# Kernel tuning notes

Hardware: AMD Instinct MI355X
Metric: run time of the kernel (lower is better)

## Reference

```python
import jax, jax.numpy as jnp
import numpy as np

E = 768
NH_REG = 6   # num_heads - cultural_heads
NH_CUL = 2   # cultural_heads


def _branch(x, wq, bq, wk, bk, wv, bv, wo, bo, cb, nh, mask_add):
    # x: [B,T,E]; weights stored as [in,out]; cb: [1,nh,1,hd]
    B, T, Edim = x.shape
    hd = Edim // nh
    scale = hd ** -0.5
    q = (x @ wq + bq).reshape(B, T, nh, hd).transpose(0, 2, 1, 3)
    k = (x @ wk + bk).reshape(B, T, nh, hd).transpose(0, 2, 1, 3)
    v = (x @ wv + bv).reshape(B, T, nh, hd).transpose(0, 2, 1, 3)
    q = q + cb  # learned cultural bias added to Q
    scores = jnp.einsum('bhtd,bhsd->bhts', q, k) * scale
    scores = scores + mask_add
    w = jax.nn.softmax(scores, axis=-1)  # dropout omitted (eval mode)
    out = jnp.einsum('bhts,bhsd->bhtd', w, v)
    out = out.transpose(0, 2, 1, 3).reshape(B, T, Edim)
    return out @ wo + bo


def setup_inputs() -> dict:
    key = jax.random.key(0)
    ks = jax.random.split(key, 24)
    B, S = 2, 2048
    d = {
        'hidden_states': jax.random.normal(ks[0], (B, S, E), jnp.float32),
        'cultural_mask': jax.random.normal(ks[1], (B, S, S), jnp.float32),
        'attention_mask': jax.random.normal(ks[2], (B, 1, 1, S), jnp.float32),
    }
    s = E ** -0.5
    names = ['rq_w', 'rk_w', 'rv_w', 'ro_w', 'cq_w', 'ck_w', 'cv_w', 'co_w']
    for i, n in enumerate(names):
        d[n] = jax.random.normal(ks[3 + i], (E, E), jnp.float32) * s
    for i, n in enumerate(['rq_b', 'rk_b', 'rv_b', 'ro_b', 'cq_b', 'ck_b', 'cv_b', 'co_b']):
        d[n] = jax.random.normal(ks[11 + i], (E,), jnp.float32) * 0.02
    d['r_cb'] = jnp.zeros((1, NH_REG, 1, E // NH_REG), jnp.float32)
    d['c_cb'] = jnp.zeros((1, NH_CUL, 1, E // NH_CUL), jnp.float32)
    # NOTE: concat of two branches gives 2E features -> out layer maps 2E -> E
    d['out_w'] = jax.random.normal(ks[19], (2 * E, E), jnp.float32) * (2 * E) ** -0.5
    d['out_b'] = jax.random.normal(ks[20], (E,), jnp.float32) * 0.02
    return d


def reference(hidden_states, cultural_mask, attention_mask,
              rq_w, rk_w, rv_w, ro_w, cq_w, ck_w, cv_w, co_w,
              rq_b, rk_b, rv_b, ro_b, cq_b, ck_b, cv_b, co_b,
              r_cb, c_cb, out_w, out_b):
    # regular branch: attention_mask only
    reg = _branch(hidden_states, rq_w, rq_b, rk_w, rk_b, rv_w, rv_b,
                  ro_w, ro_b, r_cb, NH_REG, attention_mask)
    # cultural branch: cultural_mask (broadcast over heads) + attention_mask
    cmask = cultural_mask[:, None, :, :] + attention_mask
    cul = _branch(hidden_states, cq_w, cq_b, ck_w, ck_b, cv_w, cv_b,
                  co_w, co_b, c_cb, NH_CUL, cmask)
    combined = jnp.concatenate([reg, cul], axis=-1)  # [B,T,2E]
    return combined @ out_w + out_b
```

## Files before the change

kernel.cpp:

```cpp
#include <hip/hip_runtime.h>
#include <hip/hip_bf16.h>

using u16 = unsigned short;
using u32 = unsigned int;
typedef short short8 __attribute__((ext_vector_type(8)));
typedef float f32x4 __attribute__((ext_vector_type(4)));

#define B_  2
#define S_  2048
#define E_  768
#define BS_ 4096

#define L2E_ 1.44269504088896f
#define FML2_ 17.3123404906676f

__device__ __forceinline__ u16 f2bf(float f) {
  __hip_bfloat16 h = __float2bfloat16(f);
  return *reinterpret_cast<u16*>(&h);
}

__device__ __forceinline__ u32 pk2(float a, float b) {
  return (u32)f2bf(a) | ((u32)f2bf(b) << 16);
}

__device__ __forceinline__ void gld16(const void* g, void* l) {
  __builtin_amdgcn_global_load_lds(
      (const __attribute__((address_space(1))) u32*)g,
      (__attribute__((address_space(3))) u32*)l, 16, 0, 0);
}


__global__ __launch_bounds__(256) void conv_x_k(const float* __restrict__ x,
                                                u16* __restrict__ xb, int n4) {
  int i = blockIdx.x * 256 + threadIdx.x;
  if (i >= n4) return;
  float4 v = reinterpret_cast<const float4*>(x)[i];
  reinterpret_cast<uint2*>(xb)[i] = make_uint2(pk2(v.x, v.y), pk2(v.z, v.w));
}

__global__ __launch_bounds__(256) void bias_k(
    const float* rqb, const float* rkb, const float* rvb,
    const float* cqb, const float* ckb, const float* cvb,
    const float* rob, const float* cob,
    const float* rcb, const float* ccb,
    float* bqkv, float* bproj) {
  int t = blockIdx.x * 256 + threadIdx.x;
  if (t < 4608) {
    int seg = t / 768, i = t - seg * 768;
    float v = 0.f;
    if      (seg == 0) v = rqb[i] + rcb[i];
    else if (seg == 1) v = rkb[i];
    else if (seg == 2) v = rvb[i];
    else if (seg == 3) v = cqb[i] + ccb[i];
    else if (seg == 4) v = ckb[i];
    else               v = cvb[i];
    bqkv[t] = v;
  } else {
    int u = t - 4608;
    if (u < 1536) bproj[u] = (u < 768) ? rob[u] : cob[u - 768];
  }
}

struct TP {
  const float* src[9];
  u16* dst[9];
  int rows[9];
};

__global__ __launch_bounds__(256) void transpose_k(TP p) {
  int mi = blockIdx.z;
  int rows = p.rows[mi];
  int r0 = blockIdx.y * 32;
  if (r0 >= rows) return;
  int c0 = blockIdx.x * 32;
  const float* src = p.src[mi];
  u16* dst = p.dst[mi];
  __shared__ float t[32][33];
  int tx = threadIdx.x & 31, ty = threadIdx.x >> 5;
#pragma unroll
  for (int d = 0; d < 4; ++d) {
    int r = ty + d * 8;
    t[r][tx] = src[(size_t)(r0 + r) * 768 + c0 + tx];
  }
  __syncthreads();
#pragma unroll
  for (int d = 0; d < 4; ++d) {
    int c = ty + d * 8;
    dst[(size_t)(c0 + c) * rows + r0 + tx] = f2bf(t[tx][c]);
  }
}


template<int MODE>
__global__ __launch_bounds__(256) void gemm_t_k(
    const u16* __restrict__ A, int lda,
    const u16* __restrict__ BT, int ldb,
    const float* __restrict__ bias, int K,
    const u16* __restrict__ A2, int msplit, int bofs,
    void* __restrict__ Cout, int ldc,
    u16* __restrict__ Qr, u16* __restrict__ Kr, u16* __restrict__ Vtr,
    u16* __restrict__ Qc, u16* __restrict__ Kc, u16* __restrict__ Vtc) {
  __shared__ u16 lA[128 * 32];
  __shared__ u16 lB[128 * 32];
  const int tid = threadIdx.x, w = tid >> 6, lane = tid & 63;
  const int quad = lane >> 4, l15 = lane & 15;
  const int m0 = blockIdx.y * 128, n0 = blockIdx.x * 128;
  if (msplit && m0 >= msplit) { A = A2 - (size_t)msplit * lda; BT += bofs; }

  const f32x4 z4 = {0.f, 0.f, 0.f, 0.f};
  f32x4 acc[4][4];
#pragma unroll
  for (int i = 0; i < 4; ++i)
#pragma unroll
    for (int j = 0; j < 4; ++j) acc[i][j] = z4;

  const int sr = w * 32 + (lane >> 2);
  const int scp = lane & 3;

  for (int kt = 0; kt < K; kt += 32) {
    int r1 = sr, r2 = sr + 16;
    int c1 = (scp - (r1 >> 2)) & 3;
    int c2 = (scp - (r2 >> 2)) & 3;
    gld16(A + (size_t)(m0 + r1) * lda + kt + c1 * 8, &lA[r1 * 32 + scp * 8]);
    gld16(A + (size_t)(m0 + r2) * lda + kt + c2 * 8, &lA[r2 * 32 + scp * 8]);
    gld16(BT + (size_t)(n0 + r1) * ldb + kt + c1 * 8, &lB[r1 * 32 + scp * 8]);
    gld16(BT + (size_t)(n0 + r2) * ldb + kt + c2 * 8, &lB[r2 * 32 + scp * 8]);
    __syncthreads();
    short8 af[4], bg[4];
#pragma unroll
    for (int i = 0; i < 4; ++i) {
      int r = (w >> 1) * 64 + i * 16 + l15;
      af[i] = *reinterpret_cast<const short8*>(&lA[r * 32 + ((quad + (r >> 2)) & 3) * 8]);
    }
#pragma unroll
    for (int j = 0; j < 4; ++j) {
      int r = (w & 1) * 64 + j * 16 + l15;
      bg[j] = *reinterpret_cast<const short8*>(&lB[r * 32 + ((quad + (r >> 2)) & 3) * 8]);
    }
#pragma unroll
    for (int i = 0; i < 4; ++i)
#pragma unroll
      for (int j = 0; j < 4; ++j)
        acc[i][j] = __builtin_amdgcn_mfma_f32_16x16x32_bf16(af[i], bg[j], acc[i][j], 0, 0, 0);
    __syncthreads();
  }

  const int seg = (MODE == 2) ? (m0 / 768) : 0;
#pragma unroll
  for (int i = 0; i < 4; ++i) {
    int f = m0 + (w >> 1) * 64 + i * 16 + quad * 4;
    float4 b4 = *reinterpret_cast<const float4*>(bias + f);
#pragma unroll
    for (int j = 0; j < 4; ++j) {
      int t = n0 + (w & 1) * 64 + j * 16 + l15;
      float v0 = acc[i][j][0] + b4.x;
      float v1 = acc[i][j][1] + b4.y;
      float v2 = acc[i][j][2] + b4.z;
      float v3 = acc[i][j][3] + b4.w;
      if (MODE == 0) {
        *reinterpret_cast<uint2*>((u16*)Cout + (size_t)t * ldc + f) =
            make_uint2(pk2(v0, v1), pk2(v2, v3));
      } else if (MODE == 1) {
        *reinterpret_cast<float4*>((float*)Cout + (size_t)t * ldc + f) =
            make_float4(v0, v1, v2, v3);
      } else {
        int b = t >> 11, s = t & 2047;
        int fs = f - seg * 768;
        if (seg == 0) {
          int h = fs >> 7, d = fs & 127;
          *reinterpret_cast<uint2*>(Qr + ((size_t)(b * 6 + h) * 2048 + s) * 128 + d) =
              make_uint2(pk2(v0, v1), pk2(v2, v3));
        } else if (seg == 1) {
          int h = fs >> 7, d = fs & 127;
          *reinterpret_cast<uint2*>(Kr + ((size_t)(b * 6 + h) * 2048 + s) * 128 + d) =
              make_uint2(pk2(v0, v1), pk2(v2, v3));
        } else if (seg == 2) {
          int h = fs >> 7, d = fs & 127;
          u16* vp = Vtr + ((size_t)(b * 6 + h) * 128 + d) * 2048 + s;
          vp[0] = f2bf(v0); vp[2048] = f2bf(v1); vp[4096] = f2bf(v2); vp[6144] = f2bf(v3);
        } else if (seg == 3) {
          int h = fs / 384, d = fs - h * 384;
          *reinterpret_cast<uint2*>(Qc + ((size_t)(b * 2 + h) * 2048 + s) * 384 + d) =
              make_uint2(pk2(v0, v1), pk2(v2, v3));
        } else if (seg == 4) {
          int h = fs / 384, d = fs - h * 384;
          *reinterpret_cast<uint2*>(Kc + ((size_t)(b * 2 + h) * 2048 + s) * 384 + d) =
              make_uint2(pk2(v0, v1), pk2(v2, v3));
        } else {
          int h = fs / 384, d = fs - h * 384;
          u16* vp = Vtc + ((size_t)(b * 2 + h) * 384 + d) * 2048 + s;
          vp[0] = f2bf(v0); vp[2048] = f2bf(v1); vp[4096] = f2bf(v2); vp[6144] = f2bf(v3);
        }
      }
    }
  }
}

__global__ __launch_bounds__(256) void attn_g1_k(
    const u16* __restrict__ Qr, const u16* __restrict__ Kr,
    const u16* __restrict__ Qc, const u16* __restrict__ Kc,
    u16* __restrict__ Pr, u16* __restrict__ Pc, float* __restrict__ Lp,
    const float* __restrict__ am, const float* __restrict__ cmask,
    float sReg, float sCul, int zoff) {
  __shared__ u16 lA[128 * 32];
  __shared__ u16 lB[128 * 32];
  const int tid = threadIdx.x, w = tid >> 6, lane = tid & 63;
  const int quad = lane >> 4, l15 = lane & 15;
  const int m0 = blockIdx.y * 128, n0 = blockIdx.x * 128;
  const int gz = zoff + blockIdx.z;
  const u16 *A, *BT;
  u16* P;
  const float* cm = nullptr;
  float scl;
  int K, b;
  if (gz < 12) {
    A = Kr + (size_t)gz * S_ * 128;
    BT = Qr + (size_t)gz * S_ * 128;
    K = 128;
    P = Pr + (size_t)blockIdx.z * (size_t)S_ * S_;
    scl = sReg;
    b = gz / 6;
  } else {
    int hc = gz - 12;
    A = Kc + (size_t)hc * S_ * 384;
    BT = Qc + (size_t)hc * S_ * 384;
    K = 384;
    P = Pc + (size_t)hc * (size_t)S_ * S_;
    b = hc >> 1;
    cm = cmask + (size_t)b * S_ * S_;
    scl = sCul;
  }

  const f32x4 z4 = {0.f, 0.f, 0.f, 0.f};
  f32x4 acc[4][4];
#pragma unroll
  for (int i = 0; i < 4; ++i)
#pragma unroll
    for (int j = 0; j < 4; ++j) acc[i][j] = z4;

  const int sr = w * 32 + (lane >> 2);
  const int scp = lane & 3;

  for (int kt = 0; kt < K; kt += 32) {
    int r1 = sr, r2 = sr + 16;
    int c1 = (scp - (r1 >> 2)) & 3;
    int c2 = (scp - (r2 >> 2)) & 3;
    gld16(A + (size_t)(m0 + r1) * K + kt + c1 * 8, &lA[r1 * 32 + scp * 8]);
    gld16(A + (size_t)(m0 + r2) * K + kt + c2 * 8, &lA[r2 * 32 + scp * 8]);
    gld16(BT + (size_t)(n0 + r1) * K + kt + c1 * 8, &lB[r1 * 32 + scp * 8]);
    gld16(BT + (size_t)(n0 + r2) * K + kt + c2 * 8, &lB[r2 * 32 + scp * 8]);
    __syncthreads();
    short8 af[4], bg[4];
#pragma unroll
    for (int i = 0; i < 4; ++i) {
      int r = (w >> 1) * 64 + i * 16 + l15;
      af[i] = *reinterpret_cast<const short8*>(&lA[r * 32 + ((quad + (r >> 2)) & 3) * 8]);
    }
#pragma unroll
    for (int j = 0; j < 4; ++j) {
      int r = (w & 1) * 64 + j * 16 + l15;
      bg[j] = *reinterpret_cast<const short8*>(&lB[r * 32 + ((quad + (r >> 2)) & 3) * 8]);
    }
#pragma unroll
    for (int i = 0; i < 4; ++i)
#pragma unroll
      for (int j = 0; j < 4; ++j)
        acc[i][j] = __builtin_amdgcn_mfma_f32_16x16x32_bf16(af[i], bg[j], acc[i][j], 0, 0, 0);
    __syncthreads();
  }

  const float* amb = am + b * S_;
  float lsum[4] = {0.f, 0.f, 0.f, 0.f};
#pragma unroll
  for (int i = 0; i < 4; ++i) {
    int kb = m0 + (w >> 1) * 64 + i * 16 + quad * 4;
    float4 a4 = *reinterpret_cast<const float4*>(amb + kb);
    float pre0 = fmaf(a4.x, L2E_, -FML2_);
    float pre1 = fmaf(a4.y, L2E_, -FML2_);
    float pre2 = fmaf(a4.z, L2E_, -FML2_);
    float pre3 = fmaf(a4.w, L2E_, -FML2_);
#pragma unroll
    for (int j = 0; j < 4; ++j) {
      int q = n0 + (w & 1) * 64 + j * 16 + l15;
      float c0 = pre0, c1 = pre1, c2 = pre2, c3 = pre3;
      if (cm) {
        float4 cmv = *reinterpret_cast<const float4*>(cm + (size_t)q * S_ + kb);
        c0 = fmaf(cmv.x, L2E_, c0);
        c1 = fmaf(cmv.y, L2E_, c1);
        c2 = fmaf(cmv.z, L2E_, c2);
        c3 = fmaf(cmv.w, L2E_, c3);
      }
      float p0 = exp2f(fmaf(acc[i][j][0], scl, c0));
      float p1 = exp2f(fmaf(acc[i][j][1], scl, c1));
      float p2 = exp2f(fmaf(acc[i][j][2], scl, c2));
      float p3 = exp2f(fmaf(acc[i][j][3], scl, c3));
      lsum[j] += (p0 + p1) + (p2 + p3);
      *reinterpret_cast<uint2*>(P + (size_t)q * S_ + kb) =
          make_uint2(pk2(p0, p1), pk2(p2, p3));
    }
  }
#pragma unroll
  for (int j = 0; j < 4; ++j) {
    float s = lsum[j];
    s += __shfl_xor(s, 16);
    s += __shfl_xor(s, 32);
    if (lane < 16)
      Lp[(size_t)gz * (32 * S_) + ((size_t)((m0 >> 7) * 2 + (w >> 1))) * S_ +
         n0 + (w & 1) * 64 + j * 16 + lane] = s;
  }
}

__global__ __launch_bounds__(256) void attn_g2_k(
    const u16* __restrict__ Pr, const u16* __restrict__ Pc,
    const u16* __restrict__ Vtr, const u16* __restrict__ Vtc,
    const float* __restrict__ Lp, u16* __restrict__ AO, int zoff) {
  const int gz = zoff + blockIdx.z;
  const int m0 = blockIdx.y * 128, n0 = blockIdx.x * 128;
  const u16 *A, *BT;
  int b, colbase;
  if (gz < 12) {
    if (blockIdx.y) return;
    A = Vtr + (size_t)gz * 128 * S_;
    BT = Pr + (size_t)blockIdx.z * (size_t)S_ * S_;
    b = gz / 6;
    colbase = (gz % 6) * 128;
  } else {
    int hc = gz - 12;
    A = Vtc + (size_t)hc * 384 * S_;
    BT = Pc + (size_t)hc * (size_t)S_ * S_;
    b = hc >> 1;
    colbase = 768 + (hc & 1) * 384;
  }
  __shared__ u16 lA[128 * 32];
  __shared__ u16 lB[128 * 32];
  __shared__ float lL[128];
  const int tid = threadIdx.x, w = tid >> 6, lane = tid & 63;
  const int quad = lane >> 4, l15 = lane & 15;

  if (tid < 128) {
    const float* lp = Lp + (size_t)gz * (32 * S_) + (n0 + tid);
    float s = 0.f;
#pragma unroll
    for (int g = 0; g < 32; ++g) s += lp[(size_t)g * S_];
    lL[tid] = 1.f / s;
  }

  const f32x4 z4 = {0.f, 0.f, 0.f, 0.f};
  f32x4 acc[4][4];
#pragma unroll
  for (int i = 0; i < 4; ++i)
#pragma unroll
    for (int j = 0; j < 4; ++j) acc[i][j] = z4;

  const int sr = w * 32 + (lane >> 2);
  const int scp = lane & 3;

  for (int kt = 0; kt < S_; kt += 32) {
    int r1 = sr, r2 = sr + 16;
    int c1 = (scp - (r1 >> 2)) & 3;
    int c2 = (scp - (r2 >> 2)) & 3;
    gld16(A + (size_t)(m0 + r1) * S_ + kt + c1 * 8, &lA[r1 * 32 + scp * 8]);
    gld16(A + (size_t)(m0 + r2) * S_ + kt + c2 * 8, &lA[r2 * 32 + scp * 8]);
    gld16(BT + (size_t)(n0 + r1) * S_ + kt + c1 * 8, &lB[r1 * 32 + scp * 8]);
    gld16(BT + (size_t)(n0 + r2) * S_ + kt + c2 * 8, &lB[r2 * 32 + scp * 8]);
    __syncthreads();
    short8 af[4], bg[4];
#pragma unroll
    for (int i = 0; i < 4; ++i) {
      int r = (w >> 1) * 64 + i * 16 + l15;
      af[i] = *reinterpret_cast<const short8*>(&lA[r * 32 + ((quad + (r >> 2)) & 3) * 8]);
    }
#pragma unroll
    for (int j = 0; j < 4; ++j) {
      int r = (w & 1) * 64 + j * 16 + l15;
      bg[j] = *reinterpret_cast<const short8*>(&lB[r * 32 + ((quad + (r >> 2)) & 3) * 8]);
    }
#pragma unroll
    for (int i = 0; i < 4; ++i)
#pragma unroll
      for (int j = 0; j < 4; ++j)
        acc[i][j] = __builtin_amdgcn_mfma_f32_16x16x32_bf16(af[i], bg[j], acc[i][j], 0, 0, 0);
    __syncthreads();
  }

  float invl[4];
#pragma unroll
  for (int j = 0; j < 4; ++j) invl[j] = lL[(w & 1) * 64 + j * 16 + l15];
#pragma unroll
  for (int i = 0; i < 4; ++i) {
    int feat = colbase + m0 + (w >> 1) * 64 + i * 16 + quad * 4;
#pragma unroll
    for (int j = 0; j < 4; ++j) {
      int q = n0 + (w & 1) * 64 + j * 16 + l15;
      float v0 = acc[i][j][0] * invl[j];
      float v1 = acc[i][j][1] * invl[j];
      float v2 = acc[i][j][2] * invl[j];
      float v3 = acc[i][j][3] * invl[j];
      *reinterpret_cast<uint2*>(AO + ((size_t)(b * S_ + q)) * 1536 + feat) =
          make_uint2(pk2(v0, v1), pk2(v2, v3));
    }
  }
}


extern "C" void kernel_launch(void* const* d_in, const int* in_sizes, int n_in,
                              void* d_out, int out_size, void* d_ws, size_t ws_size,
                              hipStream_t stream) {
  const float* x     = (const float*)d_in[0];
  const float* cmask = (const float*)d_in[1];
  const float* amask = (const float*)d_in[2];
  const float* W[8]  = { (const float*)d_in[3], (const float*)d_in[4], (const float*)d_in[5],
                         (const float*)d_in[6], (const float*)d_in[7], (const float*)d_in[8],
                         (const float*)d_in[9], (const float*)d_in[10] };
  const float* rq_b = (const float*)d_in[11];
  const float* rk_b = (const float*)d_in[12];
  const float* rv_b = (const float*)d_in[13];
  const float* ro_b = (const float*)d_in[14];
  const float* cq_b = (const float*)d_in[15];
  const float* ck_b = (const float*)d_in[16];
  const float* cv_b = (const float*)d_in[17];
  const float* co_b = (const float*)d_in[18];
  const float* r_cb = (const float*)d_in[19];
  const float* c_cb = (const float*)d_in[20];
  const float* out_w = (const float*)d_in[21];
  const float* out_b = (const float*)d_in[22];

  char* p = (char*)d_ws;
  auto carve = [&](size_t bytes) -> void* {
    void* r = (void*)p;
    p += (bytes + 255) & ~(size_t)255;
    return r;
  };
  u16* Xb    = (u16*)carve((size_t)BS_ * E_ * 2);
  u16* WqkvT = (u16*)carve((size_t)4608 * 768 * 2);
  u16* roT   = (u16*)carve((size_t)768 * 768 * 2);
  u16* coT   = (u16*)carve((size_t)768 * 768 * 2);
  u16* outwT = (u16*)carve((size_t)768 * 1536 * 2);
  float* bqkv  = (float*)carve(4608 * 4);
  float* bproj = (float*)carve(1536 * 4);
  u16* Qr  = (u16*)carve((size_t)B_ * 6 * S_ * 128 * 2);
  u16* Kr  = (u16*)carve((size_t)B_ * 6 * S_ * 128 * 2);
  u16* Vtr = (u16*)carve((size_t)B_ * 6 * S_ * 128 * 2);
  u16* Qc  = (u16*)carve((size_t)B_ * 2 * S_ * 384 * 2);
  u16* Kc  = (u16*)carve((size_t)B_ * 2 * S_ * 384 * 2);
  u16* Vtc = (u16*)carve((size_t)B_ * 2 * S_ * 384 * 2);
  u16* AO  = (u16*)carve((size_t)BS_ * 1536 * 2);

  float* Lp = (float*)Xb;
  u16* Pcul = (u16*)carve((size_t)4 * S_ * S_ * 2);
  size_t used = (size_t)(p - (char*)d_ws);
  size_t rem = (ws_size > used) ? (ws_size - used) : 0;
  int RCH;
  if      (rem >= (size_t)12 * S_ * S_ * 2 + 4096) RCH = 12;
  else if (rem >= (size_t)4  * S_ * S_ * 2 + 4096) RCH = 4;
  else                                             RCH = 2;
  u16* Preg = (u16*)carve((size_t)RCH * S_ * S_ * 2);
  u16* PR = Pcul;

  const float sReg = 0.08838834764831845f * L2E_;
  const float sCul = 0.05103103630798288f * L2E_;

  conv_x_k<<<dim3(BS_ * E_ / 4 / 256), 256, 0, stream>>>(x, Xb, BS_ * E_ / 4);
  bias_k<<<dim3(24), 256, 0, stream>>>(rq_b, rk_b, rv_b, cq_b, ck_b, cv_b,
                                       ro_b, co_b, r_cb, c_cb, bqkv, bproj);

  TP tp;
  const int wsel[6] = {0, 1, 2, 4, 5, 6};
  for (int i = 0; i < 6; ++i) {
    tp.src[i] = W[wsel[i]];
    tp.dst[i] = WqkvT + (size_t)i * 768 * 768;
    tp.rows[i] = 768;
  }
  tp.src[6] = W[3]; tp.dst[6] = roT;   tp.rows[6] = 768;
  tp.src[7] = W[7]; tp.dst[7] = coT;   tp.rows[7] = 768;
  tp.src[8] = out_w; tp.dst[8] = outwT; tp.rows[8] = 1536;
  transpose_k<<<dim3(24, 48, 9), 256, 0, stream>>>(tp);

  gemm_t_k<2><<<dim3(32, 36), 256, 0, stream>>>(
      WqkvT, 768, Xb, 768, bqkv, 768,
      (const u16*)nullptr, 0, 0, (void*)nullptr, 0,
      Qr, Kr, Vtr, Qc, Kc, Vtc);

  if (RCH == 12) {
    attn_g1_k<<<dim3(16, 16, 16), 256, 0, stream>>>(
        Qr, Kr, Qc, Kc, Preg, Pcul, Lp, amask, cmask, sReg, sCul, 0);
    attn_g2_k<<<dim3(16, 3, 16), 256, 0, stream>>>(
        Preg, Pcul, Vtr, Vtc, Lp, AO, 0);
  } else {
    attn_g1_k<<<dim3(16, 16, 4), 256, 0, stream>>>(
        Qr, Kr, Qc, Kc, Preg, Pcul, Lp, amask, cmask, sReg, sCul, 12);
    attn_g2_k<<<dim3(16, 3, 4), 256, 0, stream>>>(
        Preg, Pcul, Vtr, Vtc, Lp, AO, 12);
    for (int c = 0; c < 12; c += RCH) {
      attn_g1_k<<<dim3(16, 16, RCH), 256, 0, stream>>>(
          Qr, Kr, Qc, Kc, Preg, Pcul, Lp, amask, cmask, sReg, sCul, c);
      attn_g2_k<<<dim3(16, 1, RCH), 256, 0, stream>>>(
          Preg, Pcul, Vtr, Vtc, Lp, AO, c);
    }
  }

  gemm_t_k<0><<<dim3(32, 12), 256, 0, stream>>>(
      roT, 768, AO, 1536, bproj, 768,
      coT, 768, 768, (void*)PR, 1536,
      nullptr, nullptr, nullptr, nullptr, nullptr, nullptr);

  gemm_t_k<1><<<dim3(32, 6), 256, 0, stream>>>(
      outwT, 1536, PR, 1536, out_b, 1536,
      (const u16*)nullptr, 0, 0, d_out, 768,
      nullptr, nullptr, nullptr, nullptr, nullptr, nullptr);
}
```

Baseline: 403.7 us.

## Fuse QK^T softmax and PV into one flash-style attention kernel

Replaces the two-pass attention, which wrote the full bf16 probability matrix to global memory and read it back, with one kernel. Each block computes a 128-key score tile, exponentiates it into shared memory and multiplies it by V right away, accumulating row sums for normalisation at the end. This removes the large P round-trip and the Lp partial-sum buffer. The cost is that the cultural heads recompute QK^T (K=384) once for each of the three 128-column V slices, and the grid is only 16x3x16 blocks, many of which exit immediately.

```diff
diff --git a/kernel.cpp b/kernel.cpp
--- a/kernel.cpp
+++ b/kernel.cpp
@@ -196,207 +196,178 @@
   }
 }
 
-__global__ __launch_bounds__(256) void attn_g1_k(
+__global__ __launch_bounds__(256) void attn_fused_k(
     const u16* __restrict__ Qr, const u16* __restrict__ Kr,
+    const u16* __restrict__ Vtr,
     const u16* __restrict__ Qc, const u16* __restrict__ Kc,
-    u16* __restrict__ Pr, u16* __restrict__ Pc, float* __restrict__ Lp,
+    const u16* __restrict__ Vtc,
+    u16* __restrict__ AO,
     const float* __restrict__ am, const float* __restrict__ cmask,
-    float sReg, float sCul, int zoff) {
-  __shared__ u16 lA[128 * 32];
-  __shared__ u16 lB[128 * 32];
+    float sReg, float sCul) {
+  const int gz = blockIdx.z;
+  const int qt0 = blockIdx.x * 128;
+
+  const u16 *Q, *K, *Vt;
+  const float* cm = nullptr;
+  float scl;
+  int dqk, b, colbase, vrow0;
+  if (gz < 12) {
+    if (blockIdx.y) return;
+    Q  = Qr  + (size_t)gz * S_ * 128;
+    K  = Kr  + (size_t)gz * S_ * 128;
+    Vt = Vtr + (size_t)gz * 128 * S_;
+    dqk = 128; b = gz / 6; scl = sReg;
+    colbase = (gz % 6) * 128; vrow0 = 0;
+  } else {
+    const int hc = gz - 12;
+    Q  = Qc  + (size_t)hc * S_ * 384;
+    K  = Kc  + (size_t)hc * S_ * 384;
+    Vt = Vtc + (size_t)hc * 384 * S_;
+    dqk = 384; b = hc >> 1; scl = sCul;
+    cm = cmask + (size_t)b * S_ * S_;
+    vrow0 = blockIdx.y * 128;
+    colbase = 768 + (hc & 1) * 384 + vrow0;
+  }
+
+  __shared__ __align__(16) u16 lA[128 * 32];
+  __shared__ __align__(16) u16 lP[128 * 128];
+  u16* lB = lP;
+
   const int tid = threadIdx.x, w = tid >> 6, lane = tid & 63;
   const int quad = lane >> 4, l15 = lane & 15;
-  const int m0 = blockIdx.y * 128, n0 = blockIdx.x * 128;
-  const int gz = zoff + blockIdx.z;
-  const u16 *A, *BT;
-  u16* P;
-  const float* cm = nullptr;
-  float scl;
-  int K, b;
-  if (gz < 12) {
-    A = Kr + (size_t)gz * S_ * 128;
-    BT = Qr + (size_t)gz * S_ * 128;
-    K = 128;
-    P = Pr + (size_t)blockIdx.z * (size_t)S_ * S_;
-    scl = sReg;
-    b = gz / 6;
-  } else {
-    int hc = gz - 12;
-    A = Kc + (size_t)hc * S_ * 384;
-    BT = Qc + (size_t)hc * S_ * 384;
-    K = 384;
-    P = Pc + (size_t)hc * (size_t)S_ * S_;
-    b = hc >> 1;
-    cm = cmask + (size_t)b * S_ * S_;
-    scl = sCul;
-  }
-
-  const f32x4 z4 = {0.f, 0.f, 0.f, 0.f};
-  f32x4 acc[4][4];
-#pragma unroll
-  for (int i = 0; i < 4; ++i)
-#pragma unroll
-    for (int j = 0; j < 4; ++j) acc[i][j] = z4;
-
   const int sr = w * 32 + (lane >> 2);
   const int scp = lane & 3;
-
-  for (int kt = 0; kt < K; kt += 32) {
-    int r1 = sr, r2 = sr + 16;
-    int c1 = (scp - (r1 >> 2)) & 3;
-    int c2 = (scp - (r2 >> 2)) & 3;
-    gld16(A + (size_t)(m0 + r1) * K + kt + c1 * 8, &lA[r1 * 32 + scp * 8]);
-    gld16(A + (size_t)(m0 + r2) * K + kt + c2 * 8, &lA[r2 * 32 + scp * 8]);
-    gld16(BT + (size_t)(n0 + r1) * K + kt + c1 * 8, &lB[r1 * 32 + scp * 8]);
-    gld16(BT + (size_t)(n0 + r2) * K + kt + c2 * 8, &lB[r2 * 32 + scp * 8]);
+  const float* amb = am + b * S_;
+
+  const f32x4 z4 = {0.f, 0.f, 0.f, 0.f};
+  f32x4 accO[4][4];
+#pragma unroll
+  for (int i = 0; i < 4; ++i)
+#pragma unroll
+    for (int j = 0; j < 4; ++j) accO[i][j] = z4;
+  float lsum[4] = {0.f, 0.f, 0.f, 0.f};
+
+  for (int kc = 0; kc < S_; kc += 128) {
+    f32x4 accS[4][4];
+#pragma unroll
+    for (int i = 0; i < 4; ++i)
+#pragma unroll
+      for (int j = 0; j < 4; ++j) accS[i][j] = z4;
+
+    for (int kt = 0; kt < dqk; kt += 32) {
+      const int r1 = sr, r2 = sr + 16;
+      const int c1 = (scp - (r1 >> 2)) & 3;
+      const int c2 = (scp - (r2 >> 2)) & 3;
+      gld16(K + (size_t)(kc + r1) * dqk + kt + c1 * 8, &lA[r1 * 32 + scp * 8]);
+      gld16(K + (size_t)(kc + r2) * dqk + kt + c2 * 8, &lA[r2 * 32 + scp * 8]);
+      gld16(Q + (size_t)(qt0 + r1) * dqk + kt + c1 * 8, &lB[r1 * 32 + scp * 8]);
+      gld16(Q + (size_t)(qt0 + r2) * dqk + kt + c2 * 8, &lB[r2 * 32 + scp * 8]);
+      __syncthreads();
+      short8 af[4], bg[4];
+#pragma unroll
+      for (int i = 0; i < 4; ++i) {
+        int r = (w >> 1) * 64 + i * 16 + l15;
+        af[i] = *reinterpret_cast<const short8*>(&lA[r * 32 + ((quad + (r >> 2)) & 3) * 8]);
+      }
+#pragma unroll
+      for (int j = 0; j < 4; ++j) {
+        int r = (w & 1) * 64 + j * 16 + l15;
+        bg[j] = *reinterpret_cast<const short8*>(&lB[r * 32 + ((quad + (r >> 2)) & 3) * 8]);
+      }
+#pragma unroll
+      for (int i = 0; i < 4; ++i)
+#pragma unroll
+        for (int j = 0; j < 4; ++j)
+          accS[i][j] = __builtin_amdgcn_mfma_f32_16x16x32_bf16(af[i], bg[j], accS[i][j], 0, 0, 0);
+      __syncthreads();
+    }
+
+#pragma unroll
+    for (int i = 0; i < 4; ++i) {
+      const int kbl = (w >> 1) * 64 + i * 16 + quad * 4;
+      const int kg = kc + kbl;
+      float4 a4 = *reinterpret_cast<const float4*>(amb + kg);
+      float pre0 = fmaf(a4.x, L2E_, -FML2_);
+      float pre1 = fmaf(a4.y, L2E_, -FML2_);
+      float pre2 = fmaf(a4.z, L2E_, -FML2_);
+      float pre3 = fmaf(a4.w, L2E_, -FML2_);
+#pragma unroll
+      for (int j = 0; j < 4; ++j) {
+        const int ql = (w & 1) * 64 + j * 16 + l15;
+        float c0 = pre0, c1 = pre1, c2 = pre2, c3 = pre3;
+        if (cm) {
+          float4 cmv = *reinterpret_cast<const float4*>(cm + (size_t)(qt0 + ql) * S_ + kg);
+          c0 = fmaf(cmv.x, L2E_, c0);
+          c1 = fmaf(cmv.y, L2E_, c1);
+          c2 = fmaf(cmv.z, L2E_, c2);
+          c3 = fmaf(cmv.w, L2E_, c3);
+        }
+        float p0 = exp2f(fmaf(accS[i][j][0], scl, c0));
+        float p1 = exp2f(fmaf(accS[i][j][1], scl, c1));
+        float p2 = exp2f(fmaf(accS[i][j][2], scl, c2));
+        float p3 = exp2f(fmaf(accS[i][j][3], scl, c3));
+        lsum[j] += (p0 + p1) + (p2 + p3);
+        const int idx = (ql * 128 + kbl) ^ ((ql & 7) << 3);
+        *reinterpret_cast<uint2*>(&lP[idx]) = make_uint2(pk2(p0, p1), pk2(p2, p3));
+      }
+    }
     __syncthreads();
-    short8 af[4], bg[4];
-#pragma unroll
-    for (int i = 0; i < 4; ++i) {
-      int r = (w >> 1) * 64 + i * 16 + l15;
-      af[i] = *reinterpret_cast<const short8*>(&lA[r * 32 + ((quad + (r >> 2)) & 3) * 8]);
-    }
-#pragma unroll
-    for (int j = 0; j < 4; ++j) {
-      int r = (w & 1) * 64 + j * 16 + l15;
-      bg[j] = *reinterpret_cast<const short8*>(&lB[r * 32 + ((quad + (r >> 2)) & 3) * 8]);
-    }
-#pragma unroll
-    for (int i = 0; i < 4; ++i)
-#pragma unroll
-      for (int j = 0; j < 4; ++j)
-        acc[i][j] = __builtin_amdgcn_mfma_f32_16x16x32_bf16(af[i], bg[j], acc[i][j], 0, 0, 0);
-    __syncthreads();
-  }
-
-  const float* amb = am + b * S_;
-  float lsum[4] = {0.f, 0.f, 0.f, 0.f};
-#pragma unroll
-  for (int i = 0; i < 4; ++i) {
-    int kb = m0 + (w >> 1) * 64 + i * 16 + quad * 4;
-    float4 a4 = *reinterpret_cast<const float4*>(amb + kb);
-    float pre0 = fmaf(a4.x, L2E_, -FML2_);
-    float pre1 = fmaf(a4.y, L2E_, -FML2_);
-    float pre2 = fmaf(a4.z, L2E_, -FML2_);
-    float pre3 = fmaf(a4.w, L2E_, -FML2_);
-#pragma unroll
-    for (int j = 0; j < 4; ++j) {
-      int q = n0 + (w & 1) * 64 + j * 16 + l15;
-      float c0 = pre0, c1 = pre1, c2 = pre2, c3 = pre3;
-      if (cm) {
-        float4 cmv = *reinterpret_cast<const float4*>(cm + (size_t)q * S_ + kb);
-        c0 = fmaf(cmv.x, L2E_, c0);
-        c1 = fmaf(cmv.y, L2E_, c1);
-        c2 = fmaf(cmv.z, L2E_, c2);
-        c3 = fmaf(cmv.w, L2E_, c3);
-      }
-      float p0 = exp2f(fmaf(acc[i][j][0], scl, c0));
-      float p1 = exp2f(fmaf(acc[i][j][1], scl, c1));
-      float p2 = exp2f(fmaf(acc[i][j][2], scl, c2));
-      float p3 = exp2f(fmaf(acc[i][j][3], scl, c3));
-      lsum[j] += (p0 + p1) + (p2 + p3);
-      *reinterpret_cast<uint2*>(P + (size_t)q * S_ + kb) =
-          make_uint2(pk2(p0, p1), pk2(p2, p3));
-    }
-  }
+
+    for (int kt = 0; kt < 128; kt += 32) {
+      const int r1 = sr, r2 = sr + 16;
+      const int c1 = (scp - (r1 >> 2)) & 3;
+      const int c2 = (scp - (r2 >> 2)) & 3;
+      gld16(Vt + (size_t)(vrow0 + r1) * S_ + kc + kt + c1 * 8, &lA[r1 * 32 + scp * 8]);
+      gld16(Vt + (size_t)(vrow0 + r2) * S_ + kc + kt + c2 * 8, &lA[r2 * 32 + scp * 8]);
+      __syncthreads();
+      short8 af[4], bg[4];
+#pragma unroll
+      for (int i = 0; i < 4; ++i) {
+        int r = (w >> 1) * 64 + i * 16 + l15;
+        af[i] = *reinterpret_cast<const short8*>(&lA[r * 32 + ((quad + (r >> 2)) & 3) * 8]);
+      }
+#pragma unroll
+      for (int j = 0; j < 4; ++j) {
+        int r = (w & 1) * 64 + j * 16 + l15;
+        int idx = (r * 128 + kt + quad * 8) ^ ((r & 7) << 3);
+        bg[j] = *reinterpret_cast<const short8*>(&lP[idx]);
+      }
+#pragma unroll
+      for (int i = 0; i < 4; ++i)
+#pragma unroll
+        for (int j = 0; j < 4; ++j)
+          accO[i][j] = __builtin_amdgcn_mfma_f32_16x16x32_bf16(af[i], bg[j], accO[i][j], 0, 0, 0);
+      __syncthreads();
+    }
+  }
+
+  float* lSum = reinterpret_cast<float*>(lA);
 #pragma unroll
   for (int j = 0; j < 4; ++j) {
     float s = lsum[j];
     s += __shfl_xor(s, 16);
     s += __shfl_xor(s, 32);
-    if (lane < 16)
-      Lp[(size_t)gz * (32 * S_) + ((size_t)((m0 >> 7) * 2 + (w >> 1))) * S_ +
-         n0 + (w & 1) * 64 + j * 16 + lane] = s;
-  }
-}
-
-__global__ __launch_bounds__(256) void attn_g2_k(
-    const u16* __restrict__ Pr, const u16* __restrict__ Pc,
-    const u16* __restrict__ Vtr, const u16* __restrict__ Vtc,
-    const float* __restrict__ Lp, u16* __restrict__ AO, int zoff) {
-  const int gz = zoff + blockIdx.z;
-  const int m0 = blockIdx.y * 128, n0 = blockIdx.x * 128;
-  const u16 *A, *BT;
-  int b, colbase;
-  if (gz < 12) {
-    if (blockIdx.y) return;
-    A = Vtr + (size_t)gz * 128 * S_;
-    BT = Pr + (size_t)blockIdx.z * (size_t)S_ * S_;
-    b = gz / 6;
-    colbase = (gz % 6) * 128;
-  } else {
-    int hc = gz - 12;
-    A = Vtc + (size_t)hc * 384 * S_;
-    BT = Pc + (size_t)hc * (size_t)S_ * S_;
-    b = hc >> 1;
-    colbase = 768 + (hc & 1) * 384;
-  }
-  __shared__ u16 lA[128 * 32];
-  __shared__ u16 lB[128 * 32];
-  __shared__ float lL[128];
-  const int tid = threadIdx.x, w = tid >> 6, lane = tid & 63;
-  const int quad = lane >> 4, l15 = lane & 15;
-
-  if (tid < 128) {
-    const float* lp = Lp + (size_t)gz * (32 * S_) + (n0 + tid);
-    float s = 0.f;
-#pragma unroll
-    for (int g = 0; g < 32; ++g) s += lp[(size_t)g * S_];
-    lL[tid] = 1.f / s;
-  }
-
-  const f32x4 z4 = {0.f, 0.f, 0.f, 0.f};
-  f32x4 acc[4][4];
-#pragma unroll
-  for (int i = 0; i < 4; ++i)
-#pragma unroll
-    for (int j = 0; j < 4; ++j) acc[i][j] = z4;
-
-  const int sr = w * 32 + (lane >> 2);
-  const int scp = lane & 3;
-
-  for (int kt = 0; kt < S_; kt += 32) {
-    int r1 = sr, r2 = sr + 16;
-    int c1 = (scp - (r1 >> 2)) & 3;
-    int c2 = (scp - (r2 >> 2)) & 3;
-    gld16(A + (size_t)(m0 + r1) * S_ + kt + c1 * 8, &lA[r1 * 32 + scp * 8]);
-    gld16(A + (size_t)(m0 + r2) * S_ + kt + c2 * 8, &lA[r2 * 32 + scp * 8]);
-    gld16(BT + (size_t)(n0 + r1) * S_ + kt + c1 * 8, &lB[r1 * 32 + scp * 8]);
-    gld16(BT + (size_t)(n0 + r2) * S_ + kt + c2 * 8, &lB[r2 * 32 + scp * 8]);
-    __syncthreads();
-    short8 af[4], bg[4];
-#pragma unroll
-    for (int i = 0; i < 4; ++i) {
-      int r = (w >> 1) * 64 + i * 16 + l15;
-      af[i] = *reinterpret_cast<const short8*>(&lA[r * 32 + ((quad + (r >> 2)) & 3) * 8]);
-    }
+    if (lane < 16) lSum[(w >> 1) * 128 + (w & 1) * 64 + j * 16 + lane] = s;
+  }
+  __syncthreads();
+  float invl[4];
+#pragma unroll
+  for (int j = 0; j < 4; ++j) {
+    const int ql = (w & 1) * 64 + j * 16 + l15;
+    invl[j] = 1.f / (lSum[ql] + lSum[128 + ql]);
+  }
+
+#pragma unroll
+  for (int i = 0; i < 4; ++i) {
+    const int feat = colbase + (w >> 1) * 64 + i * 16 + quad * 4;
 #pragma unroll
     for (int j = 0; j < 4; ++j) {
-      int r = (w & 1) * 64 + j * 16 + l15;
-      bg[j] = *reinterpret_cast<const short8*>(&lB[r * 32 + ((quad + (r >> 2)) & 3) * 8]);
-    }
-#pragma unroll
-    for (int i = 0; i < 4; ++i)
-#pragma unroll
-      for (int j = 0; j < 4; ++j)
-        acc[i][j] = __builtin_amdgcn_mfma_f32_16x16x32_bf16(af[i], bg[j], acc[i][j], 0, 0, 0);
-    __syncthreads();
-  }
-
-  float invl[4];
-#pragma unroll
-  for (int j = 0; j < 4; ++j) invl[j] = lL[(w & 1) * 64 + j * 16 + l15];
-#pragma unroll
-  for (int i = 0; i < 4; ++i) {
-    int feat = colbase + m0 + (w >> 1) * 64 + i * 16 + quad * 4;
-#pragma unroll
-    for (int j = 0; j < 4; ++j) {
-      int q = n0 + (w & 1) * 64 + j * 16 + l15;
-      float v0 = acc[i][j][0] * invl[j];
-      float v1 = acc[i][j][1] * invl[j];
-      float v2 = acc[i][j][2] * invl[j];
-      float v3 = acc[i][j][3] * invl[j];
-      *reinterpret_cast<uint2*>(AO + ((size_t)(b * S_ + q)) * 1536 + feat) =
+      const int qg = qt0 + (w & 1) * 64 + j * 16 + l15;
+      float v0 = accO[i][j][0] * invl[j];
+      float v1 = accO[i][j][1] * invl[j];
+      float v2 = accO[i][j][2] * invl[j];
+      float v3 = accO[i][j][3] * invl[j];
+      *reinterpret_cast<uint2*>(AO + ((size_t)(b * S_ + qg)) * 1536 + feat) =
           make_uint2(pk2(v0, v1), pk2(v2, v3));
     }
   }
@@ -445,17 +416,7 @@
   u16* Kc  = (u16*)carve((size_t)B_ * 2 * S_ * 384 * 2);
   u16* Vtc = (u16*)carve((size_t)B_ * 2 * S_ * 384 * 2);
   u16* AO  = (u16*)carve((size_t)BS_ * 1536 * 2);
-
-  float* Lp = (float*)Xb;
-  u16* Pcul = (u16*)carve((size_t)4 * S_ * S_ * 2);
-  size_t used = (size_t)(p - (char*)d_ws);
-  size_t rem = (ws_size > used) ? (ws_size - used) : 0;
-  int RCH;
-  if      (rem >= (size_t)12 * S_ * S_ * 2 + 4096) RCH = 12;
-  else if (rem >= (size_t)4  * S_ * S_ * 2 + 4096) RCH = 4;
-  else                                             RCH = 2;
-  u16* Preg = (u16*)carve((size_t)RCH * S_ * S_ * 2);
-  u16* PR = Pcul;
+  u16* PR  = (u16*)carve((size_t)BS_ * 1536 * 2);
 
   const float sReg = 0.08838834764831845f * L2E_;
   const float sCul = 0.05103103630798288f * L2E_;
@@ -481,23 +442,8 @@
       (const u16*)nullptr, 0, 0, (void*)nullptr, 0,
       Qr, Kr, Vtr, Qc, Kc, Vtc);
 
-  if (RCH == 12) {
-    attn_g1_k<<<dim3(16, 16, 16), 256, 0, stream>>>(
-        Qr, Kr, Qc, Kc, Preg, Pcul, Lp, amask, cmask, sReg, sCul, 0);
-    attn_g2_k<<<dim3(16, 3, 16), 256, 0, stream>>>(
-        Preg, Pcul, Vtr, Vtc, Lp, AO, 0);
-  } else {
-    attn_g1_k<<<dim3(16, 16, 4), 256, 0, stream>>>(
-        Qr, Kr, Qc, Kc, Preg, Pcul, Lp, amask, cmask, sReg, sCul, 12);
-    attn_g2_k<<<dim3(16, 3, 4), 256, 0, stream>>>(
-        Preg, Pcul, Vtr, Vtc, Lp, AO, 12);
-    for (int c = 0; c < 12; c += RCH) {
-      attn_g1_k<<<dim3(16, 16, RCH), 256, 0, stream>>>(
-          Qr, Kr, Qc, Kc, Preg, Pcul, Lp, amask, cmask, sReg, sCul, c);
-      attn_g2_k<<<dim3(16, 1, RCH), 256, 0, stream>>>(
-          Preg, Pcul, Vtr, Vtc, Lp, AO, c);
-    }
-  }
+  attn_fused_k<<<dim3(16, 3, 16), 256, 0, stream>>>(
+      Qr, Kr, Vtr, Qc, Kc, Vtc, AO, amask, cmask, sReg, sCul);
 
   gemm_t_k<0><<<dim3(32, 12), 256, 0, stream>>>(
       roT, 768, AO, 1536, bproj, 768,
```

Result: slower. 638.3 us (+58.1%).

## Fold per-branch output projections into final output weight, merge prep kernels

Applied to the files above, without the earlier changes.

Premultiplies each branch's output-projection weight by the matching half of the final output weight, producing a fused 1536x768 weight and a fused bias. This removes the per-call 4096x1536x768 projection GEMM and its intermediate buffer, at the cost of a small weight-only GEMM (768x768 per branch) and a bias reduction done every call. The conversion, transpose and bias kernels are also merged into one launch. Rounding the fused weight to bf16 changes numerics slightly.

```diff
diff --git a/kernel.cpp b/kernel.cpp
--- a/kernel.cpp
+++ b/kernel.cpp
@@ -29,64 +29,75 @@
       (__attribute__((address_space(3))) u32*)l, 16, 0, 0);
 }
 
-
-__global__ __launch_bounds__(256) void conv_x_k(const float* __restrict__ x,
-                                                u16* __restrict__ xb, int n4) {
-  int i = blockIdx.x * 256 + threadIdx.x;
-  if (i >= n4) return;
-  float4 v = reinterpret_cast<const float4*>(x)[i];
-  reinterpret_cast<uint2*>(xb)[i] = make_uint2(pk2(v.x, v.y), pk2(v.z, v.w));
-}
-
-__global__ __launch_bounds__(256) void bias_k(
-    const float* rqb, const float* rkb, const float* rvb,
-    const float* cqb, const float* ckb, const float* cvb,
-    const float* rob, const float* cob,
-    const float* rcb, const float* ccb,
-    float* bqkv, float* bproj) {
-  int t = blockIdx.x * 256 + threadIdx.x;
-  if (t < 4608) {
-    int seg = t / 768, i = t - seg * 768;
-    float v = 0.f;
-    if      (seg == 0) v = rqb[i] + rcb[i];
-    else if (seg == 1) v = rkb[i];
-    else if (seg == 2) v = rvb[i];
-    else if (seg == 3) v = cqb[i] + ccb[i];
-    else if (seg == 4) v = ckb[i];
-    else               v = cvb[i];
-    bqkv[t] = v;
+struct PrepP {
+  const float* x;  u16* Xb;
+  const float* row; const float* cow; u16* Wrc;
+  const float* tsrc[7]; u16* tdst[7]; int trows[7];
+  const float* rqb; const float* rkb; const float* rvb;
+  const float* cqb; const float* ckb; const float* cvb;
+  const float* rcb; const float* ccb;
+  float* bqkv; float* bzero;
+  const float* out_w; const float* out_b;
+  const float* ro_b; const float* co_b; float* bfused;
+};
+
+__global__ __launch_bounds__(256) void prep_k(PrepP p) {
+  const int bid = blockIdx.x, tid = threadIdx.x;
+  __shared__ float tsh[32][33];
+  if (bid < 3072) {
+    int i = bid * 256 + tid;
+    float4 v = reinterpret_cast<const float4*>(p.x)[i];
+    reinterpret_cast<uint2*>(p.Xb)[i] = make_uint2(pk2(v.x, v.y), pk2(v.z, v.w));
+  } else if (bid < 4224) {
+    int i = (bid - 3072) * 256 + tid;
+    const float* s = (i < 147456) ? p.row : p.cow;
+    int k = (i < 147456) ? i : i - 147456;
+    float4 v = reinterpret_cast<const float4*>(s)[k];
+    reinterpret_cast<uint2*>(p.Wrc)[i] = make_uint2(pk2(v.x, v.y), pk2(v.z, v.w));
+  } else if (bid < 8832) {
+    int tb = bid - 4224;
+    int mi, ty, tx;
+    if (tb < 3456) { mi = tb / 576; int r = tb - mi * 576; ty = r / 24; tx = r - ty * 24; }
+    else           { int r = tb - 3456; mi = 6; ty = r / 24; tx = r - ty * 24; }
+    const float* src = p.tsrc[mi];
+    u16* dst = p.tdst[mi];
+    const int rows = p.trows[mi];
+    const int r0 = ty * 32, c0 = tx * 32;
+    const int txx = tid & 31, tyy = tid >> 5;
+#pragma unroll
+    for (int d = 0; d < 4; ++d) {
+      int r = tyy + d * 8;
+      tsh[r][txx] = src[(size_t)(r0 + r) * 768 + c0 + txx];
+    }
+    __syncthreads();
+#pragma unroll
+    for (int d = 0; d < 4; ++d) {
+      int c = tyy + d * 8;
+      dst[(size_t)(c0 + c) * rows + r0 + txx] = f2bf(tsh[txx][c]);
+    }
+  } else if (bid < 8856) {
+    int t = (bid - 8832) * 256 + tid;
+    if (t < 4608) {
+      int seg = t / 768, i = t - seg * 768;
+      float v = 0.f;
+      if      (seg == 0) v = p.rqb[i] + p.rcb[i];
+      else if (seg == 1) v = p.rkb[i];
+      else if (seg == 2) v = p.rvb[i];
+      else if (seg == 3) v = p.cqb[i] + p.ccb[i];
+      else if (seg == 4) v = p.ckb[i];
+      else               v = p.cvb[i];
+      p.bqkv[t] = v;
+    } else if (t < 6144) {
+      p.bzero[t - 4608] = 0.f;
+    }
   } else {
-    int u = t - 4608;
-    if (u < 1536) bproj[u] = (u < 768) ? rob[u] : cob[u - 768];
-  }
-}
-
-struct TP {
-  const float* src[9];
-  u16* dst[9];
-  int rows[9];
-};
-
-__global__ __launch_bounds__(256) void transpose_k(TP p) {
-  int mi = blockIdx.z;
-  int rows = p.rows[mi];
-  int r0 = blockIdx.y * 32;
-  if (r0 >= rows) return;
-  int c0 = blockIdx.x * 32;
-  const float* src = p.src[mi];
-  u16* dst = p.dst[mi];
-  __shared__ float t[32][33];
-  int tx = threadIdx.x & 31, ty = threadIdx.x >> 5;
-#pragma unroll
-  for (int d = 0; d < 4; ++d) {
-    int r = ty + d * 8;
-    t[r][tx] = src[(size_t)(r0 + r) * 768 + c0 + tx];
-  }
-  __syncthreads();
-#pragma unroll
-  for (int d = 0; d < 4; ++d) {
-    int c = ty + d * 8;
-    dst[(size_t)(c0 + c) * rows + r0 + tx] = f2bf(t[tx][c]);
+    int of = (bid - 8856) * 256 + tid;
+    float acc = p.out_b[of];
+#pragma unroll 4
+    for (int m = 0; m < 768; ++m)
+      acc = fmaf(p.ro_b[m], p.out_w[(size_t)m * 768 + of],
+            fmaf(p.co_b[m], p.out_w[(size_t)(768 + m) * 768 + of], acc));
+    p.bfused[of] = acc;
   }
 }
 
@@ -433,11 +444,12 @@
   };
   u16* Xb    = (u16*)carve((size_t)BS_ * E_ * 2);
   u16* WqkvT = (u16*)carve((size_t)4608 * 768 * 2);
-  u16* roT   = (u16*)carve((size_t)768 * 768 * 2);
-  u16* coT   = (u16*)carve((size_t)768 * 768 * 2);
   u16* outwT = (u16*)carve((size_t)768 * 1536 * 2);
-  float* bqkv  = (float*)carve(4608 * 4);
-  float* bproj = (float*)carve(1536 * 4);
+  u16* Wrc   = (u16*)carve((size_t)1536 * 768 * 2);
+  u16* WfT   = (u16*)carve((size_t)768 * 1536 * 2);
+  float* bqkv   = (float*)carve(4608 * 4);
+  float* bzero  = (float*)carve(1536 * 4);
+  float* bfused = (float*)carve(768 * 4);
   u16* Qr  = (u16*)carve((size_t)B_ * 6 * S_ * 128 * 2);
   u16* Kr  = (u16*)carve((size_t)B_ * 6 * S_ * 128 * 2);
   u16* Vtr = (u16*)carve((size_t)B_ * 6 * S_ * 128 * 2);
@@ -455,26 +467,32 @@
   else if (rem >= (size_t)4  * S_ * S_ * 2 + 4096) RCH = 4;
   else                                             RCH = 2;
   u16* Preg = (u16*)carve((size_t)RCH * S_ * S_ * 2);
-  u16* PR = Pcul;
 
   const float sReg = 0.08838834764831845f * L2E_;
   const float sCul = 0.05103103630798288f * L2E_;
 
-  conv_x_k<<<dim3(BS_ * E_ / 4 / 256), 256, 0, stream>>>(x, Xb, BS_ * E_ / 4);
-  bias_k<<<dim3(24), 256, 0, stream>>>(rq_b, rk_b, rv_b, cq_b, ck_b, cv_b,
-                                       ro_b, co_b, r_cb, c_cb, bqkv, bproj);
-
-  TP tp;
+  PrepP pp;
+  pp.x = x; pp.Xb = Xb;
+  pp.row = W[3]; pp.cow = W[7]; pp.Wrc = Wrc;
   const int wsel[6] = {0, 1, 2, 4, 5, 6};
   for (int i = 0; i < 6; ++i) {
-    tp.src[i] = W[wsel[i]];
-    tp.dst[i] = WqkvT + (size_t)i * 768 * 768;
-    tp.rows[i] = 768;
-  }
-  tp.src[6] = W[3]; tp.dst[6] = roT;   tp.rows[6] = 768;
-  tp.src[7] = W[7]; tp.dst[7] = coT;   tp.rows[7] = 768;
-  tp.src[8] = out_w; tp.dst[8] = outwT; tp.rows[8] = 1536;
-  transpose_k<<<dim3(24, 48, 9), 256, 0, stream>>>(tp);
+    pp.tsrc[i] = W[wsel[i]];
+    pp.tdst[i] = WqkvT + (size_t)i * 768 * 768;
+    pp.trows[i] = 768;
+  }
+  pp.tsrc[6] = out_w; pp.tdst[6] = outwT; pp.trows[6] = 1536;
+  pp.rqb = rq_b; pp.rkb = rk_b; pp.rvb = rv_b;
+  pp.cqb = cq_b; pp.ckb = ck_b; pp.cvb = cv_b;
+  pp.rcb = r_cb; pp.ccb = c_cb;
+  pp.bqkv = bqkv; pp.bzero = bzero;
+  pp.out_w = out_w; pp.out_b = out_b;
+  pp.ro_b = ro_b; pp.co_b = co_b; pp.bfused = bfused;
+  prep_k<<<dim3(8859), 256, 0, stream>>>(pp);
+
+  gemm_t_k<0><<<dim3(6, 12), 256, 0, stream>>>(
+      Wrc, 768, outwT, 1536, bzero, 768,
+      Wrc + (size_t)768 * 768, 768, 768, (void*)WfT, 1536,
+      nullptr, nullptr, nullptr, nullptr, nullptr, nullptr);
 
   gemm_t_k<2><<<dim3(32, 36), 256, 0, stream>>>(
       WqkvT, 768, Xb, 768, bqkv, 768,
@@ -499,13 +517,8 @@
     }
   }
 
-  gemm_t_k<0><<<dim3(32, 12), 256, 0, stream>>>(
-      roT, 768, AO, 1536, bproj, 768,
-      coT, 768, 768, (void*)PR, 1536,
-      nullptr, nullptr, nullptr, nullptr, nullptr, nullptr);
-
   gemm_t_k<1><<<dim3(32, 6), 256, 0, stream>>>(
-      outwT, 1536, PR, 1536, out_b, 1536,
+      WfT, 1536, AO, 1536, bfused, 1536,
       (const u16*)nullptr, 0, 0, d_out, 768,
       nullptr, nullptr, nullptr, nullptr, nullptr, nullptr);
 }
```

Result: slower. 462.7 us (+14.6%).
